# Kernel tuning notes

Measured on AMD Instinct MI355X. Metric: run time of the kernel, lower is better.

The kernel has to match this reference:

```python
import jax, jax.numpy as jnp
import numpy as np

B, N, E, D, L, V = 8, 10000, 160000, 128, 4, 100000


def setup_inputs() -> dict:
    key = jax.random.key(0)
    ks = jax.random.split(key, 10)
    s = 1.0 / np.sqrt(D)
    x = jax.random.randint(ks[0], (B, N, 1), 0, V, dtype=jnp.int32)
    edge_index = jax.random.randint(ks[1], (B, 2, E), 0, N, dtype=jnp.int32)
    embed_w = jax.random.normal(ks[2], (V, D), jnp.float32) * 0.1
    ggnn_w = jax.random.normal(ks[3], (L, D, D), jnp.float32) * s  # per-layer linear
    W_ih = jax.random.normal(ks[4], (3 * D, D), jnp.float32) * s   # GRUCell input weights (r,z,n)
    W_hh = jax.random.normal(ks[5], (3 * D, D), jnp.float32) * s   # GRUCell hidden weights
    b_ih = jax.random.normal(ks[6], (3 * D,), jnp.float32) * s
    b_hh = jax.random.normal(ks[7], (3 * D,), jnp.float32) * s
    gate_w = jax.random.normal(ks[8], (D, 1), jnp.float32) * s     # mlp_gate Linear(d,1)
    gate_b = jax.random.normal(ks[9], (1,), jnp.float32) * s
    return dict(x=x, edge_index=edge_index, embed_w=embed_w, ggnn_w=ggnn_w,
                W_ih=W_ih, W_hh=W_hh, b_ih=b_ih, b_hh=b_hh,
                gate_w=gate_w, gate_b=gate_b)


def reference(x, edge_index, embed_w, ggnn_w, W_ih, W_hh, b_ih, b_hh, gate_w, gate_b):
    h0 = embed_w[x[..., 0]]  # [B, N, D] embedding lookup (squeeze(1))

    def per_graph(h, ei):
        src, dst = ei[0], ei[1]
        n_nodes = h.shape[0]

        def layer(h, w):
            m = h @ w                                             # [N, D] per-layer linear
            agg = jax.ops.segment_sum(m[src], dst, num_segments=n_nodes)  # scatter-add messages
            # GRUCell(agg, h), torch gate order: r, z, n
            gi = agg @ W_ih.T + b_ih
            gh = h @ W_hh.T + b_hh
            ir, iz, inn = jnp.split(gi, 3, axis=-1)
            hr, hz, hn = jnp.split(gh, 3, axis=-1)
            r = jax.nn.sigmoid(ir + hr)
            z = jax.nn.sigmoid(iz + hz)
            n = jnp.tanh(inn + r * hn)
            return (1.0 - z) * n + z * h, None

        h, _ = jax.lax.scan(layer, h, ggnn_w)
        # GlobalAttention: gate = sigmoid(Linear(h)), softmax over nodes, weighted sum
        gate = jax.nn.sigmoid(h @ gate_w + gate_b)  # [N, 1]
        att = jax.nn.softmax(gate, axis=0)
        return jnp.sum(att * h, axis=0)             # [D]

    return jax.vmap(per_graph)(h0, edge_index)      # [B, D]
```

## Files before the change

### kernel.cpp

```cpp
#include <hip/hip_runtime.h>
#include <hip/hip_bf16.h>
#include <math.h>

#define BGR 8
#define NND 10000
#define EDG 160000
#define DIM 128
#define LAY 4
#define BN (BGR * NND)
#define CSTR 516

typedef short bf16x8 __attribute__((ext_vector_type(8)));
typedef float f32x4 __attribute__((ext_vector_type(4)));
typedef unsigned int uint;
typedef unsigned short ushort;

__device__ __forceinline__ float bf2f(ushort h) {
    return __uint_as_float(((uint)h) << 16);
}
__device__ __forceinline__ ushort f2bf(float f) {
    uint u = __float_as_uint(f);
    u += 0x7FFFu + ((u >> 16) & 1u);
    return (ushort)(u >> 16);
}
__device__ __forceinline__ uint pack2(float lo, float hi) {
    return (uint)f2bf(lo) | ((uint)f2bf(hi) << 16);
}
__device__ __forceinline__ void split8(const float* __restrict__ p,
                                       bf16x8& hi, bf16x8& lo) {
    float4 v0 = *reinterpret_cast<const float4*>(p);
    float4 v1 = *reinterpret_cast<const float4*>(p + 4);
    float a[8] = {v0.x, v0.y, v0.z, v0.w, v1.x, v1.y, v1.z, v1.w};
    #pragma unroll
    for (int e = 0; e < 8; ++e) {
        ushort h = f2bf(a[e]);
        hi[e] = (short)h;
        lo[e] = (short)f2bf(a[e] - bf2f(h));
    }
}

__global__ void k_embed(const int* __restrict__ x, const float* __restrict__ emb,
                        float* __restrict__ Hf, ushort* __restrict__ Hb) {
    int t = blockIdx.x * 256 + threadIdx.x;
    int row = t >> 5, l = t & 31;
    if (row >= BN) return;
    int idx = x[row];
    float4 v = *reinterpret_cast<const float4*>(emb + (size_t)idx * DIM + l * 4);
    *reinterpret_cast<float4*>(Hf + (size_t)row * DIM + l * 4) = v;
    uint2 o;
    o.x = pack2(v.x, v.y);
    o.y = pack2(v.z, v.w);
    *reinterpret_cast<uint2*>(Hb + (size_t)row * DIM + l * 4) = o;
}

__global__ __launch_bounds__(256) void k_wmul(const float* __restrict__ ggnn,
                                              const float* __restrict__ Wih,
                                              float* __restrict__ Mw) {
    __shared__ float Bs[16][129];
    int lay = blockIdx.x / 24, jt = blockIdx.x % 24;
    int j0 = jt * 16;
    int t = threadIdx.x;
    {
        int j = t >> 4, c0 = (t & 15) * 8;
        float4 v0 = *reinterpret_cast<const float4*>(&Wih[(size_t)(j0 + j) * 128 + c0]);
        float4 v1 = *reinterpret_cast<const float4*>(&Wih[(size_t)(j0 + j) * 128 + c0 + 4]);
        Bs[j][c0+0]=v0.x; Bs[j][c0+1]=v0.y; Bs[j][c0+2]=v0.z; Bs[j][c0+3]=v0.w;
        Bs[j][c0+4]=v1.x; Bs[j][c0+5]=v1.y; Bs[j][c0+6]=v1.z; Bs[j][c0+7]=v1.w;
    }
    __syncthreads();
    const float* A = ggnn + (size_t)lay * 128 * 128;
    int j = t & 15;
    int r8 = (t >> 4) * 8;
    float acc[8] = {};
    for (int c = 0; c < 128; ++c) {
        float bv = Bs[j][c];
        #pragma unroll
        for (int i = 0; i < 8; ++i)
            acc[i] += A[(size_t)(r8 + i) * 128 + c] * bv;
    }
    #pragma unroll
    for (int i = 0; i < 8; ++i)
        Mw[((size_t)lay * 128 + r8 + i) * 384 + j0 + j] = acc[i];
}

__global__ void k_packb(const float* __restrict__ Mw, const float* __restrict__ Whh,
                        ushort* __restrict__ Bhi, ushort* __restrict__ Blo) {
    int g = blockIdx.x * 256 + threadIdx.x;
    if (g >= 4 * 131072) return;
    int lay = g >> 17, rem = g & 131071;
    int e = rem & 7, lane = (rem >> 3) & 63, ctg = (rem >> 9) & 31, kt = rem >> 14;
    int k = kt * 32 + (lane >> 4) * 8 + e;
    int j = ctg * 16 + (lane & 15);
    float v;
    if (k < 128) {
        v = (j < 384) ? Mw[((size_t)lay * 128 + k) * 384 + j] : 0.f;
    } else {
        int kk = k - 128;
        if (j < 256)      v = Whh[(size_t)j * 128 + kk];
        else if (j < 384) v = 0.f;
        else              v = Whh[(size_t)(j - 128) * 128 + kk];
    }
    ushort h = f2bf(v);
    Bhi[g] = h;
    Blo[g] = f2bf(v - bf2f(h));
}

__global__ void k_bias(const float* __restrict__ bih, const float* __restrict__ bhh,
                       float* __restrict__ biasc) {
    int j = threadIdx.x;
    if (j < 512)
        biasc[j] = (j < 256) ? bih[j] + bhh[j] : ((j < 384) ? bih[j] : bhh[j - 128]);
}

__global__ void k_deg(const int* __restrict__ ei, int* __restrict__ deg) {
    int t = blockIdx.x * 256 + threadIdx.x;
    if (t >= BGR * EDG) return;
    int b = t / EDG, e = t % EDG;
    int dst = ei[((size_t)b * 2 + 1) * EDG + e];
    atomicAdd(&deg[b * NND + dst], 1);
}

__global__ void k_scan(const int* __restrict__ deg, int* __restrict__ offs,
                       int* __restrict__ cur) {
    __shared__ int s[256];
    __shared__ int runsh;
    int b = blockIdx.x, t = threadIdx.x;
    if (t == 0) runsh = 0;
    __syncthreads();
    for (int n0 = 0; n0 < NND; n0 += 256) {
        int n = n0 + t;
        int d = (n < NND) ? deg[b * NND + n] : 0;
        s[t] = d;
        __syncthreads();
        for (int off = 1; off < 256; off <<= 1) {
            int add = (t >= off) ? s[t - off] : 0;
            __syncthreads();
            s[t] += add;
            __syncthreads();
        }
        int base = runsh;
        int excl = s[t] - d;
        if (n < NND) {
            offs[b * (NND + 1) + n] = base + excl;
            cur[b * NND + n] = base + excl;
        }
        int tot = s[255];
        __syncthreads();
        if (t == 0) runsh = base + tot;
        __syncthreads();
    }
    if (t == 0) offs[b * (NND + 1) + NND] = runsh;
}

__global__ void k_fill(const int* __restrict__ ei, int* __restrict__ cur,
                       int* __restrict__ csr) {
    int t = blockIdx.x * 256 + threadIdx.x;
    if (t >= BGR * EDG) return;
    int b = t / EDG, e = t % EDG;
    int src = ei[((size_t)b * 2 + 0) * EDG + e];
    int dst = ei[((size_t)b * 2 + 1) * EDG + e];
    int pos = atomicAdd(&cur[b * NND + dst], 1);
    csr[(size_t)b * EDG + pos] = src;
}

__global__ void k_agg(const ushort* __restrict__ HB, const int* __restrict__ offs,
                      const int* __restrict__ csr, float* __restrict__ AGF) {
    int wid = (blockIdx.x * blockDim.x + threadIdx.x) >> 6;
    int lane = threadIdx.x & 63;
    if (wid >= BN) return;
    int b = wid / NND, n = wid - b * NND;
    int s0 = offs[b * (NND + 1) + n], s1 = offs[b * (NND + 1) + n + 1];
    int q = lane >> 4, l = lane & 15;
    const int* cs = csr + (size_t)b * EDG;
    const ushort* Hbase = HB + (size_t)b * NND * DIM;
    float a0[8] = {}, a1[8] = {};
    int e = s0 + q;
    for (; e + 4 < s1; e += 8) {
        int sA = cs[e], sB = cs[e + 4];
        uint4 vA = *reinterpret_cast<const uint4*>(Hbase + (size_t)sA * DIM + l * 8);
        uint4 vB = *reinterpret_cast<const uint4*>(Hbase + (size_t)sB * DIM + l * 8);
        a0[0] += bf2f((ushort)(vA.x & 0xFFFF)); a0[1] += bf2f((ushort)(vA.x >> 16));
        a0[2] += bf2f((ushort)(vA.y & 0xFFFF)); a0[3] += bf2f((ushort)(vA.y >> 16));
        a0[4] += bf2f((ushort)(vA.z & 0xFFFF)); a0[5] += bf2f((ushort)(vA.z >> 16));
        a0[6] += bf2f((ushort)(vA.w & 0xFFFF)); a0[7] += bf2f((ushort)(vA.w >> 16));
        a1[0] += bf2f((ushort)(vB.x & 0xFFFF)); a1[1] += bf2f((ushort)(vB.x >> 16));
        a1[2] += bf2f((ushort)(vB.y & 0xFFFF)); a1[3] += bf2f((ushort)(vB.y >> 16));
        a1[4] += bf2f((ushort)(vB.z & 0xFFFF)); a1[5] += bf2f((ushort)(vB.z >> 16));
        a1[6] += bf2f((ushort)(vB.w & 0xFFFF)); a1[7] += bf2f((ushort)(vB.w >> 16));
    }
    if (e < s1) {
        int sA = cs[e];
        uint4 vA = *reinterpret_cast<const uint4*>(Hbase + (size_t)sA * DIM + l * 8);
        a0[0] += bf2f((ushort)(vA.x & 0xFFFF)); a0[1] += bf2f((ushort)(vA.x >> 16));
        a0[2] += bf2f((ushort)(vA.y & 0xFFFF)); a0[3] += bf2f((ushort)(vA.y >> 16));
        a0[4] += bf2f((ushort)(vA.z & 0xFFFF)); a0[5] += bf2f((ushort)(vA.z >> 16));
        a0[6] += bf2f((ushort)(vA.w & 0xFFFF)); a0[7] += bf2f((ushort)(vA.w >> 16));
    }
    #pragma unroll
    for (int i = 0; i < 8; ++i) {
        float v = a0[i] + a1[i];
        v += __shfl_xor(v, 16, 64);
        v += __shfl_xor(v, 32, 64);
        a0[i] = v;
    }
    if (q == 0) {
        float4 o0 = {a0[0], a0[1], a0[2], a0[3]};
        float4 o1 = {a0[4], a0[5], a0[6], a0[7]};
        *reinterpret_cast<float4*>(AGF + (size_t)wid * DIM + l * 8) = o0;
        *reinterpret_cast<float4*>(AGF + (size_t)wid * DIM + l * 8 + 4) = o1;
    }
}

__global__ __launch_bounds__(512) void k_gru(const float* __restrict__ AGF,
                                             const ushort* __restrict__ Bhi,
                                             const ushort* __restrict__ Blo,
                                             const float* __restrict__ biasc,
                                             float* __restrict__ Hf,
                                             ushort* __restrict__ HBn) {
    __shared__ float Cs[16][CSTR];
    int t = threadIdx.x;
    int w = t >> 6, l = t & 63;
    int i0 = blockIdx.x * 16;
    int lrow = l & 15, lgrp = l >> 4;
    f32x4 acc[4] = {{0.f,0.f,0.f,0.f},{0.f,0.f,0.f,0.f},{0.f,0.f,0.f,0.f},{0.f,0.f,0.f,0.f}};
    int kt_lo = (w >= 6) ? 4 : 0;
    int kt_hi = (w == 4 || w == 5) ? 4 : 8;
    const size_t arow = (size_t)(i0 + lrow) * DIM;
    for (int kt = kt_lo; kt < kt_hi; ++kt) {
        const float* asrc = (kt < 4) ? AGF : Hf;
        int kk = (kt & 3) * 32 + lgrp * 8;
        bf16x8 ahi, alo;
        split8(asrc + arow + kk, ahi, alo);
        #pragma unroll
        for (int ct = 0; ct < 4; ++ct) {
            int ctg = w * 4 + ct;
            size_t boff = (((size_t)kt * 32 + ctg) * 64 + l) * 8;
            bf16x8 bh = *reinterpret_cast<const bf16x8*>(Bhi + boff);
            bf16x8 bl = *reinterpret_cast<const bf16x8*>(Blo + boff);
            acc[ct] = __builtin_amdgcn_mfma_f32_16x16x32_bf16(ahi, bh, acc[ct], 0, 0, 0);
            acc[ct] = __builtin_amdgcn_mfma_f32_16x16x32_bf16(ahi, bl, acc[ct], 0, 0, 0);
            acc[ct] = __builtin_amdgcn_mfma_f32_16x16x32_bf16(alo, bh, acc[ct], 0, 0, 0);
        }
    }
    #pragma unroll
    for (int ct = 0; ct < 4; ++ct) {
        int c = w * 64 + ct * 16 + lrow;
        #pragma unroll
        for (int r = 0; r < 4; ++r)
            Cs[lgrp * 4 + r][c] = acc[ct][r];
    }
    __syncthreads();
    int d = t & 127;
    int r0 = t >> 7;
    #pragma unroll
    for (int i = 0; i < 4; ++i) {
        int r = r0 * 4 + i;
        float cr = Cs[r][d]       + biasc[d];
        float cz = Cs[r][128 + d] + biasc[128 + d];
        float cn = Cs[r][256 + d] + biasc[256 + d];
        float ch = Cs[r][384 + d] + biasc[384 + d];
        float rr = 1.f / (1.f + __expf(-cr));
        float zz = 1.f / (1.f + __expf(-cz));
        float nn = tanhf(cn + rr * ch);
        size_t idx = (size_t)(i0 + r) * DIM + d;
        float hp = Hf[idx];
        float hv = (1.f - zz) * nn + zz * hp;
        Hf[idx] = hv;
        HBn[idx] = f2bf(hv);
    }
}

__global__ void k_gate(const float* __restrict__ H, const float* __restrict__ gw,
                       const float* __restrict__ gb, float* __restrict__ gates) {
    int wid = (blockIdx.x * blockDim.x + threadIdx.x) >> 6;
    int lane = threadIdx.x & 63;
    if (wid >= BN) return;
    float v = H[(size_t)wid * 128 + lane] * gw[lane] +
              H[(size_t)wid * 128 + 64 + lane] * gw[64 + lane];
    for (int off = 32; off; off >>= 1) v += __shfl_xor(v, off, 64);
    if (lane == 0) {
        float g = 1.f / (1.f + expf(-(v + gb[0])));
        gates[wid] = expf(g);
    }
}

__global__ __launch_bounds__(256) void k_pool(const float* __restrict__ H,
                                              const float* __restrict__ gates,
                                              float* __restrict__ pacc,
                                              float* __restrict__ wsum) {
    __shared__ float red[256];
    const int chunks = (NND + 127) / 128;
    int b = blockIdx.x / chunks;
    int n0 = (blockIdx.x % chunks) * 128;
    int nend = min(n0 + 128, NND);
    int t = threadIdx.x;
    int d = t & 127, half = t >> 7;
    float acc = 0.f, asum = 0.f;
    for (int n = n0 + half; n < nend; n += 2)
        acc += gates[b * NND + n] * H[((size_t)b * NND + n) * 128 + d];
    for (int n = n0 + t; n < nend; n += 256)
        asum += gates[b * NND + n];
    red[t] = acc;
    __syncthreads();
    if (half == 0) atomicAdd(&pacc[b * 128 + d], red[t] + red[t + 128]);
    for (int off = 32; off; off >>= 1) asum += __shfl_xor(asum, off, 64);
    __syncthreads();
    if ((t & 63) == 0) red[t >> 6] = asum;
    __syncthreads();
    if (t == 0) atomicAdd(&wsum[b], red[0] + red[1] + red[2] + red[3]);
}

__global__ void k_final(const float* __restrict__ pacc, const float* __restrict__ wsum,
                        float* __restrict__ out) {
    int t = blockIdx.x * 256 + threadIdx.x;
    if (t >= BGR * 128) return;
    out[t] = pacc[t] / wsum[t >> 7];
}

extern "C" void kernel_launch(void* const* d_in, const int* in_sizes, int n_in,
                              void* d_out, int out_size, void* d_ws, size_t ws_size,
                              hipStream_t stream) {
    const int*   x    = (const int*)d_in[0];
    const int*   ei   = (const int*)d_in[1];
    const float* embw = (const float*)d_in[2];
    const float* ggnn = (const float*)d_in[3];
    const float* Wih  = (const float*)d_in[4];
    const float* Whh  = (const float*)d_in[5];
    const float* bih  = (const float*)d_in[6];
    const float* bhh  = (const float*)d_in[7];
    const float* gw   = (const float*)d_in[8];
    const float* gb   = (const float*)d_in[9];
    float* out = (float*)d_out;

    char* base = (char*)d_ws;
    size_t off = 0;
    auto alloc = [&](size_t bytes) -> void* {
        void* p = base + off;
        off = (off + bytes + 255) & ~(size_t)255;
        return p;
    };
    float*  Hf    = (float*)alloc((size_t)BN * DIM * 4);
    float*  AGF   = (float*)alloc((size_t)BN * DIM * 4);
    ushort* Hb    = (ushort*)alloc((size_t)BN * DIM * 2);
    float*  Mw    = (float*)alloc((size_t)LAY * 128 * 384 * 4);
    ushort* Bhi   = (ushort*)alloc((size_t)LAY * 131072 * 2);
    ushort* Blo   = (ushort*)alloc((size_t)LAY * 131072 * 2);
    float*  biasc = (float*)alloc(512 * 4);
    int*    deg   = (int*)alloc((size_t)BGR * NND * 4);
    int*    offs  = (int*)alloc((size_t)BGR * (NND + 1) * 4);
    int*    cur   = (int*)alloc((size_t)BGR * NND * 4);
    int*    csr   = (int*)alloc((size_t)BGR * EDG * 4);
    float*  gates = (float*)alloc((size_t)BGR * NND * 4);
    float*  pacc  = (float*)alloc(BGR * 128 * 4 + 256);
    float*  wsum  = pacc + BGR * 128;
    if (off > ws_size) return;

    hipMemsetAsync(deg, 0, (size_t)BGR * NND * 4, stream);
    hipMemsetAsync(pacc, 0, BGR * 128 * 4 + 64, stream);

    k_embed<<<(BN * 32) / 256, 256, 0, stream>>>(x, embw, Hf, Hb);
    k_wmul<<<LAY * 24, 256, 0, stream>>>(ggnn, Wih, Mw);
    k_packb<<<(LAY * 131072) / 256, 256, 0, stream>>>(Mw, Whh, Bhi, Blo);
    k_bias<<<1, 512, 0, stream>>>(bih, bhh, biasc);
    k_deg<<<(BGR * EDG) / 256, 256, 0, stream>>>(ei, deg);
    k_scan<<<BGR, 256, 0, stream>>>(deg, offs, cur);
    k_fill<<<(BGR * EDG) / 256, 256, 0, stream>>>(ei, cur, csr);

    for (int l = 0; l < LAY; ++l) {
        k_agg<<<BN / 4, 256, 0, stream>>>(Hb, offs, csr, AGF);
        k_gru<<<BN / 16, 512, 0, stream>>>(AGF, Bhi + (size_t)l * 131072,
                                           Blo + (size_t)l * 131072,
                                           biasc, Hf, Hb);
    }

    k_gate<<<BN / 4, 256, 0, stream>>>(Hf, gw, gb, gates);
    k_pool<<<BGR * ((NND + 127) / 128), 256, 0, stream>>>(Hf, gates, pacc, wsum);
    k_final<<<(BGR * 128 + 255) / 256, 256, 0, stream>>>(pacc, wsum, out);
}
```

Measured before the change: 993.8 us.

## Retile GRU GEMM to 64 rows per block with in-register gate epilogue

The GRU kernel now processes 64 rows per block instead of 16. Each wave owns 16 output columns across all four gate groups (r, z, n_input, n_hidden), so the B fragments are reused across four row tiles and the gate math runs directly from accumulator registers, without a shared-memory staging buffer. The degree scan is also changed from a serial chunked loop to a per-thread partial sum followed by a single block scan. The cost is more accumulator registers per thread (launch bounds of 512 with 4 set), reduced block count, and A-row loads repeated per wave.

```diff
diff --git a/kernel.cpp b/kernel.cpp
--- a/kernel.cpp
+++ b/kernel.cpp
@@ -8,7 +8,6 @@
 #define DIM 128
 #define LAY 4
 #define BN (BGR * NND)
-#define CSTR 516
 
 typedef short bf16x8 __attribute__((ext_vector_type(8)));
 typedef float f32x4 __attribute__((ext_vector_type(4)));
@@ -123,33 +122,33 @@
 __global__ void k_scan(const int* __restrict__ deg, int* __restrict__ offs,
                        int* __restrict__ cur) {
     __shared__ int s[256];
-    __shared__ int runsh;
     int b = blockIdx.x, t = threadIdx.x;
-    if (t == 0) runsh = 0;
-    __syncthreads();
-    for (int n0 = 0; n0 < NND; n0 += 256) {
-        int n = n0 + t;
-        int d = (n < NND) ? deg[b * NND + n] : 0;
-        s[t] = d;
+    const int PER = (NND + 255) / 256;
+    int n0 = t * PER;
+    const int* dg = deg + b * NND;
+    int sum = 0;
+    for (int i = 0; i < PER; ++i) {
+        int n = n0 + i;
+        if (n < NND) sum += dg[n];
+    }
+    s[t] = sum;
+    __syncthreads();
+    for (int off = 1; off < 256; off <<= 1) {
+        int add = (t >= off) ? s[t - off] : 0;
         __syncthreads();
-        for (int off = 1; off < 256; off <<= 1) {
-            int add = (t >= off) ? s[t - off] : 0;
-            __syncthreads();
-            s[t] += add;
-            __syncthreads();
+        s[t] += add;
+        __syncthreads();
+    }
+    int run = (t == 0) ? 0 : s[t - 1];
+    for (int i = 0; i < PER; ++i) {
+        int n = n0 + i;
+        if (n < NND) {
+            offs[b * (NND + 1) + n] = run;
+            cur[b * NND + n] = run;
+            run += dg[n];
         }
-        int base = runsh;
-        int excl = s[t] - d;
-        if (n < NND) {
-            offs[b * (NND + 1) + n] = base + excl;
-            cur[b * NND + n] = base + excl;
-        }
-        int tot = s[255];
-        __syncthreads();
-        if (t == 0) runsh = base + tot;
-        __syncthreads();
-    }
-    if (t == 0) offs[b * (NND + 1) + NND] = runsh;
+    }
+    if (t == 255) offs[b * (NND + 1) + NND] = s[255];
 }
 
 __global__ void k_fill(const int* __restrict__ ei, int* __restrict__ cur,
@@ -211,62 +210,75 @@
     }
 }
 
-__global__ __launch_bounds__(512) void k_gru(const float* __restrict__ AGF,
-                                             const ushort* __restrict__ Bhi,
-                                             const ushort* __restrict__ Blo,
-                                             const float* __restrict__ biasc,
-                                             float* __restrict__ Hf,
-                                             ushort* __restrict__ HBn) {
-    __shared__ float Cs[16][CSTR];
+__global__ __launch_bounds__(512, 4) void k_gru(const float* __restrict__ AGF,
+                                                const ushort* __restrict__ Bhi,
+                                                const ushort* __restrict__ Blo,
+                                                const float* __restrict__ biasc,
+                                                float* __restrict__ Hf,
+                                                ushort* __restrict__ HBn) {
     int t = threadIdx.x;
     int w = t >> 6, l = t & 63;
-    int i0 = blockIdx.x * 16;
     int lrow = l & 15, lgrp = l >> 4;
-    f32x4 acc[4] = {{0.f,0.f,0.f,0.f},{0.f,0.f,0.f,0.f},{0.f,0.f,0.f,0.f},{0.f,0.f,0.f,0.f}};
-    int kt_lo = (w >= 6) ? 4 : 0;
-    int kt_hi = (w == 4 || w == 5) ? 4 : 8;
-    const size_t arow = (size_t)(i0 + lrow) * DIM;
-    for (int kt = kt_lo; kt < kt_hi; ++kt) {
+    int i0 = blockIdx.x * 64;
+    int d = w * 16 + lrow;
+    float bs0 = biasc[d], bs1 = biasc[128 + d], bs2 = biasc[256 + d], bs3 = biasc[384 + d];
+    f32x4 acc0[4] = {{0,0,0,0},{0,0,0,0},{0,0,0,0},{0,0,0,0}};
+    f32x4 acc1[4] = {{0,0,0,0},{0,0,0,0},{0,0,0,0},{0,0,0,0}};
+    f32x4 acc2[4] = {{0,0,0,0},{0,0,0,0},{0,0,0,0},{0,0,0,0}};
+    f32x4 acc3[4] = {{0,0,0,0},{0,0,0,0},{0,0,0,0},{0,0,0,0}};
+    for (int kt = 0; kt < 8; ++kt) {
         const float* asrc = (kt < 4) ? AGF : Hf;
         int kk = (kt & 3) * 32 + lgrp * 8;
-        bf16x8 ahi, alo;
-        split8(asrc + arow + kk, ahi, alo);
+        int ctgC = (kt < 4) ? (w + 16) : (w + 24);
+        size_t bo0 = (((size_t)kt * 32 + (w))      * 64 + l) * 8;
+        size_t bo1 = (((size_t)kt * 32 + (w + 8))  * 64 + l) * 8;
+        size_t boC = (((size_t)kt * 32 + ctgC)     * 64 + l) * 8;
+        bf16x8 bh0 = *reinterpret_cast<const bf16x8*>(Bhi + bo0);
+        bf16x8 bl0 = *reinterpret_cast<const bf16x8*>(Blo + bo0);
+        bf16x8 bh1 = *reinterpret_cast<const bf16x8*>(Bhi + bo1);
+        bf16x8 bl1 = *reinterpret_cast<const bf16x8*>(Blo + bo1);
+        bf16x8 bhC = *reinterpret_cast<const bf16x8*>(Bhi + boC);
+        bf16x8 blC = *reinterpret_cast<const bf16x8*>(Blo + boC);
         #pragma unroll
-        for (int ct = 0; ct < 4; ++ct) {
-            int ctg = w * 4 + ct;
-            size_t boff = (((size_t)kt * 32 + ctg) * 64 + l) * 8;
-            bf16x8 bh = *reinterpret_cast<const bf16x8*>(Bhi + boff);
-            bf16x8 bl = *reinterpret_cast<const bf16x8*>(Blo + boff);
-            acc[ct] = __builtin_amdgcn_mfma_f32_16x16x32_bf16(ahi, bh, acc[ct], 0, 0, 0);
-            acc[ct] = __builtin_amdgcn_mfma_f32_16x16x32_bf16(ahi, bl, acc[ct], 0, 0, 0);
-            acc[ct] = __builtin_amdgcn_mfma_f32_16x16x32_bf16(alo, bh, acc[ct], 0, 0, 0);
+        for (int rt = 0; rt < 4; ++rt) {
+            bf16x8 ahi, alo;
+            split8(asrc + (size_t)(i0 + rt * 16 + lrow) * DIM + kk, ahi, alo);
+            acc0[rt] = __builtin_amdgcn_mfma_f32_16x16x32_bf16(ahi, bh0, acc0[rt], 0, 0, 0);
+            acc0[rt] = __builtin_amdgcn_mfma_f32_16x16x32_bf16(ahi, bl0, acc0[rt], 0, 0, 0);
+            acc0[rt] = __builtin_amdgcn_mfma_f32_16x16x32_bf16(alo, bh0, acc0[rt], 0, 0, 0);
+            acc1[rt] = __builtin_amdgcn_mfma_f32_16x16x32_bf16(ahi, bh1, acc1[rt], 0, 0, 0);
+            acc1[rt] = __builtin_amdgcn_mfma_f32_16x16x32_bf16(ahi, bl1, acc1[rt], 0, 0, 0);
+            acc1[rt] = __builtin_amdgcn_mfma_f32_16x16x32_bf16(alo, bh1, acc1[rt], 0, 0, 0);
+            if (kt < 4) {
+                acc2[rt] = __builtin_amdgcn_mfma_f32_16x16x32_bf16(ahi, bhC, acc2[rt], 0, 0, 0);
+                acc2[rt] = __builtin_amdgcn_mfma_f32_16x16x32_bf16(ahi, blC, acc2[rt], 0, 0, 0);
+                acc2[rt] = __builtin_amdgcn_mfma_f32_16x16x32_bf16(alo, bhC, acc2[rt], 0, 0, 0);
+            } else {
+                acc3[rt] = __builtin_amdgcn_mfma_f32_16x16x32_bf16(ahi, bhC, acc3[rt], 0, 0, 0);
+                acc3[rt] = __builtin_amdgcn_mfma_f32_16x16x32_bf16(ahi, blC, acc3[rt], 0, 0, 0);
+                acc3[rt] = __builtin_amdgcn_mfma_f32_16x16x32_bf16(alo, bhC, acc3[rt], 0, 0, 0);
+            }
         }
     }
+    __syncthreads();
     #pragma unroll
-    for (int ct = 0; ct < 4; ++ct) {
-        int c = w * 64 + ct * 16 + lrow;
+    for (int rt = 0; rt < 4; ++rt) {
         #pragma unroll
-        for (int r = 0; r < 4; ++r)
-            Cs[lgrp * 4 + r][c] = acc[ct][r];
-    }
-    __syncthreads();
-    int d = t & 127;
-    int r0 = t >> 7;
-    #pragma unroll
-    for (int i = 0; i < 4; ++i) {
-        int r = r0 * 4 + i;
-        float cr = Cs[r][d]       + biasc[d];
-        float cz = Cs[r][128 + d] + biasc[128 + d];
-        float cn = Cs[r][256 + d] + biasc[256 + d];
-        float ch = Cs[r][384 + d] + biasc[384 + d];
-        float rr = 1.f / (1.f + __expf(-cr));
-        float zz = 1.f / (1.f + __expf(-cz));
-        float nn = tanhf(cn + rr * ch);
-        size_t idx = (size_t)(i0 + r) * DIM + d;
-        float hp = Hf[idx];
-        float hv = (1.f - zz) * nn + zz * hp;
-        Hf[idx] = hv;
-        HBn[idx] = f2bf(hv);
+        for (int r = 0; r < 4; ++r) {
+            int row = i0 + rt * 16 + lgrp * 4 + r;
+            float cr = acc0[rt][r] + bs0;
+            float cz = acc1[rt][r] + bs1;
+            float cn = acc2[rt][r] + bs2;
+            float ch = acc3[rt][r] + bs3;
+            float rr = 1.f / (1.f + __expf(-cr));
+            float zz = 1.f / (1.f + __expf(-cz));
+            float nn = tanhf(cn + rr * ch);
+            size_t idx = (size_t)row * DIM + d;
+            float hp = Hf[idx];
+            float hv = (1.f - zz) * nn + zz * hp;
+            Hf[idx] = hv;
+            HBn[idx] = f2bf(hv);
+        }
     }
 }
 
@@ -368,7 +380,7 @@
 
     for (int l = 0; l < LAY; ++l) {
         k_agg<<<BN / 4, 256, 0, stream>>>(Hb, offs, csr, AGF);
-        k_gru<<<BN / 16, 512, 0, stream>>>(AGF, Bhi + (size_t)l * 131072,
+        k_gru<<<BN / 64, 512, 0, stream>>>(AGF, Bhi + (size_t)l * 131072,
                                            Blo + (size_t)l * 131072,
                                            biasc, Hf, Hb);
     }
```

Result: faster. 939.3 us (-5.5%).
